# Kernel optimization log

Hardware: AMD Instinct MI355X
Metric: run time of the kernel (lower is better)

Reference implementation:

```python
import jax, jax.numpy as jnp
import numpy as np

B = 131072
D = 256  # embedding_dim
P = 64   # prosody / accent feature dim

# per-speaker prosody constants from the hardcoded 4-speaker table
PITCH_TAB = jnp.array([120.0, 100.0, 220.0, 190.0], dtype=jnp.float32) / 200.0
ENERGY_TAB = jnp.array([0.8, 0.6, 0.85, 0.7], dtype=jnp.float32)
RATE_TAB = jnp.array([1.1, 0.9, 1.15, 1.0], dtype=jnp.float32)


def setup_inputs() -> dict:
    key = jax.random.key(0)
    ks = jax.random.split(key, 16)
    s = 0.05
    return {
        "speaker_id": jax.random.randint(ks[0], (B,), 0, 4, dtype=jnp.int64),
        "emotion_embedding": jax.random.normal(ks[1], (B, D), dtype=jnp.float32),
        "accent_level": 1,
        "emb_table": jax.random.normal(ks[2], (4, D), dtype=jnp.float32),
        "pitch_w": jax.random.normal(ks[3], (P,), dtype=jnp.float32) * s,
        "pitch_b": jax.random.normal(ks[4], (P,), dtype=jnp.float32) * s,
        "energy_w": jax.random.normal(ks[5], (P,), dtype=jnp.float32) * s,
        "energy_b": jax.random.normal(ks[6], (P,), dtype=jnp.float32) * s,
        "rate_w": jax.random.normal(ks[7], (P,), dtype=jnp.float32) * s,
        "rate_b": jax.random.normal(ks[8], (P,), dtype=jnp.float32) * s,
        "accent_table": jax.random.normal(ks[9], (3, P), dtype=jnp.float32),
        "w1": jax.random.normal(ks[10], (D + 3 * P + P, D), dtype=jnp.float32) * s,
        "b1": jnp.zeros((D,), dtype=jnp.float32),
        "ln_g": jnp.ones((D,), dtype=jnp.float32),
        "ln_b": jnp.zeros((D,), dtype=jnp.float32),
        "w2": jax.random.normal(ks[11], (D, D), dtype=jnp.float32) * s,
        "b2": jnp.zeros((D,), dtype=jnp.float32),
        "emo_w": jax.random.normal(ks[12], (D, D), dtype=jnp.float32) * s,
        "emo_b": jnp.zeros((D,), dtype=jnp.float32),
    }


def reference(speaker_id, emotion_embedding, accent_level, emb_table,
              pitch_w, pitch_b, energy_w, energy_b, rate_w, rate_b,
              accent_table, w1, b1, ln_g, ln_b, w2, b2, emo_w, emo_b):
    b = speaker_id.shape[0]
    speaker_embed = emb_table[speaker_id]  # [B, D]
    # vectorized replacement of the per-sample prosody loop: Linear(1,64) == outer product
    pitch_feat = PITCH_TAB[speaker_id][:, None] * pitch_w[None, :] + pitch_b
    energy_feat = ENERGY_TAB[speaker_id][:, None] * energy_w[None, :] + energy_b
    rate_feat = RATE_TAB[speaker_id][:, None] * rate_w[None, :] + rate_b
    prosody = jnp.concatenate([pitch_feat, energy_feat, rate_feat], axis=1)  # [B, 192]
    accent_embed = jnp.broadcast_to(accent_table[accent_level][None, :], (b, P))
    combined = jnp.concatenate([speaker_embed, prosody, accent_embed], axis=1)  # [B, 512]
    h = jax.nn.relu(combined @ w1 + b1)
    # LayerNorm (eps=1e-5)
    mu = jnp.mean(h, axis=-1, keepdims=True)
    var = jnp.mean(jnp.square(h - mu), axis=-1, keepdims=True)
    h = (h - mu) * jax.lax.rsqrt(var + 1e-5) * ln_g + ln_b
    out = h @ w2 + b2
    out = out + 0.3 * (emotion_embedding @ emo_w + emo_b)
    # F.normalize(dim=-1)
    norm = jnp.maximum(jnp.linalg.norm(out, axis=-1, keepdims=True), 1e-12)
    return out / norm
```

## Files before the change

### kernel.cpp

```cpp
#include <hip/hip_runtime.h>
#include <hip/hip_bf16.h>

typedef __attribute__((ext_vector_type(8))) short bf16x8;
typedef __attribute__((ext_vector_type(4))) float f32x4;

static __device__ inline short f2bf(float f) {
    __hip_bfloat16 h = __float2bfloat16(f);
    return *reinterpret_cast<short*>(&h);
}

__global__ __launch_bounds__(1024) void setup_kernel(
    const float* __restrict__ emb_table,
    const float* __restrict__ pitch_w, const float* __restrict__ pitch_b,
    const float* __restrict__ energy_w, const float* __restrict__ energy_b,
    const float* __restrict__ rate_w, const float* __restrict__ rate_b,
    const float* __restrict__ accent_table, const int* __restrict__ accent_level,
    const float* __restrict__ w1, const float* __restrict__ b1,
    const float* __restrict__ ln_g, const float* __restrict__ ln_b,
    const float* __restrict__ w2, const float* __restrict__ b2,
    const float* __restrict__ emo_w, const float* __restrict__ emo_b,
    float* __restrict__ base_out, unsigned short* __restrict__ wpack)
{
    if (blockIdx.x < 4) {
        const int s = blockIdx.x;
        __shared__ float comb[512];
        __shared__ float part[4][256];
        __shared__ float redS[16];
        __shared__ float redQ[16];
        __shared__ float hbuf[256];
        const int t = threadIdx.x;
        const int n = t & 255;
        const int kp = t >> 8;

        if (t < 512) {
            const int i = t;
            float v;
            if (i < 256) {
                v = emb_table[s * 256 + i];
            } else if (i < 320) {
                float pt = (s == 0) ? 0.6f : (s == 1) ? 0.5f : (s == 2) ? 1.1f : 0.95f;
                v = pt * pitch_w[i - 256] + pitch_b[i - 256];
            } else if (i < 384) {
                float et = (s == 0) ? 0.8f : (s == 1) ? 0.6f : (s == 2) ? 0.85f : 0.7f;
                v = et * energy_w[i - 320] + energy_b[i - 320];
            } else if (i < 448) {
                float rt = (s == 0) ? 1.1f : (s == 1) ? 0.9f : (s == 2) ? 1.15f : 1.0f;
                v = rt * rate_w[i - 384] + rate_b[i - 384];
            } else {
                v = accent_table[accent_level[0] * 64 + (i - 448)];
            }
            comb[i] = v;
        }
        __syncthreads();

        float hp = 0.f;
        {
            const int k0 = kp * 128;
            #pragma unroll 8
            for (int k = 0; k < 128; ++k)
                hp = fmaf(comb[k0 + k], w1[(size_t)(k0 + k) * 256 + n], hp);
        }
        part[kp][n] = hp;
        __syncthreads();

        float h = b1[n] + part[0][n] + part[1][n] + part[2][n] + part[3][n];
        h = fmaxf(h, 0.f);

        float sum = h, sq = h * h;
        for (int m = 32; m; m >>= 1) {
            sum += __shfl_xor(sum, m, 64);
            sq  += __shfl_xor(sq, m, 64);
        }
        if ((t & 63) == 0) { redS[t >> 6] = sum; redQ[t >> 6] = sq; }
        __syncthreads();
        const float tot = redS[0] + redS[1] + redS[2] + redS[3];
        const float tsq = redQ[0] + redQ[1] + redQ[2] + redQ[3];
        const float mu  = tot * (1.0f / 256.0f);
        const float var = tsq * (1.0f / 256.0f) - mu * mu;
        const float hn = (h - mu) * rsqrtf(var + 1e-5f) * ln_g[n] + ln_b[n];
        if (t < 256) hbuf[n] = hn;
        __syncthreads();

        float op = 0.f;
        {
            const int k0 = kp * 64;
            #pragma unroll 8
            for (int k = 0; k < 64; ++k)
                op = fmaf(hbuf[k0 + k], w2[(size_t)(k0 + k) * 256 + n], op);
        }
        part[kp][n] = op;
        __syncthreads();
        if (t < 256) {
            base_out[s * 256 + n] = b2[n] + 0.3f * emo_b[n]
                                  + part[0][n] + part[1][n] + part[2][n] + part[3][n];
        }
    } else {
        const int idx = (blockIdx.x - 4) * 1024 + threadIdx.x;
        const int l  = idx & 63;
        const int ks = (idx >> 6) & 7;
        const int ct = idx >> 9;
        const int col = ct * 16 + (l & 15);
        const int kb  = ks * 32 + (l >> 4) * 8;
        bf16x8 pk;
        #pragma unroll
        for (int j = 0; j < 8; ++j) pk[j] = f2bf(emo_w[(size_t)(kb + j) * 256 + col]);
        *reinterpret_cast<bf16x8*>(wpack + (size_t)idx * 8) = pk;
    }
}

__global__ __launch_bounds__(1024) void main_kernel(
    const float* __restrict__ emo, const int* __restrict__ sid,
    const float* __restrict__ base, const unsigned short* __restrict__ wpack,
    float* __restrict__ out)
{
    extern __shared__ unsigned short sB[];
    const int tid = threadIdx.x;

    #pragma unroll
    for (int p = 0; p < 8; ++p) {
        const int e = p * 1024 + tid;
        *reinterpret_cast<bf16x8*>(sB + e * 8) =
            *reinterpret_cast<const bf16x8*>(wpack + (size_t)e * 8);
    }
    __syncthreads();

    const int wave = tid >> 6;
    const int lane = tid & 63;
    const int row0 = blockIdx.x * 256 + wave * 16;
    const int arow = lane & 15;
    const int agrp = lane >> 4;

    const float* aptr = emo + (size_t)(row0 + arow) * 256 + agrp * 8;
    const unsigned short* bptr = sB + lane * 8;

    f32x4 acc[16];
    const f32x4 zero = {0.f, 0.f, 0.f, 0.f};
    #pragma unroll
    for (int i = 0; i < 16; ++i) acc[i] = zero;

    #pragma unroll
    for (int ks = 0; ks < 8; ++ks) {
        f32x4 a0 = *reinterpret_cast<const f32x4*>(aptr + ks * 32);
        f32x4 a1 = *reinterpret_cast<const f32x4*>(aptr + ks * 32 + 4);
        bf16x8 af;
        af[0] = f2bf(a0[0]); af[1] = f2bf(a0[1]); af[2] = f2bf(a0[2]); af[3] = f2bf(a0[3]);
        af[4] = f2bf(a1[0]); af[5] = f2bf(a1[1]); af[6] = f2bf(a1[2]); af[7] = f2bf(a1[3]);
        #pragma unroll
        for (int ct = 0; ct < 16; ++ct) {
            bf16x8 bfr = *reinterpret_cast<const bf16x8*>(bptr + ((ct * 8 + ks) << 9));
            acc[ct] = __builtin_amdgcn_mfma_f32_16x16x32_bf16(af, bfr, acc[ct], 0, 0, 0);
        }
    }

    int sidv[4];
    #pragma unroll
    for (int j = 0; j < 4; ++j) sidv[j] = sid[row0 + agrp * 4 + j];

    float p[4] = {0.f, 0.f, 0.f, 0.f};
    #pragma unroll
    for (int ct = 0; ct < 16; ++ct) {
        #pragma unroll
        for (int j = 0; j < 4; ++j) {
            float pre = fmaf(0.3f, acc[ct][j], base[sidv[j] * 256 + ct * 16 + arow]);
            acc[ct][j] = pre;
            p[j] = fmaf(pre, pre, p[j]);
        }
    }
    #pragma unroll
    for (int j = 0; j < 4; ++j) {
        p[j] += __shfl_xor(p[j], 1, 64);
        p[j] += __shfl_xor(p[j], 2, 64);
        p[j] += __shfl_xor(p[j], 4, 64);
        p[j] += __shfl_xor(p[j], 8, 64);
        float nrm = fmaxf(sqrtf(p[j]), 1e-12f);
        p[j] = 1.0f / nrm;
    }
    #pragma unroll
    for (int ct = 0; ct < 16; ++ct) {
        #pragma unroll
        for (int j = 0; j < 4; ++j) {
            out[(size_t)(row0 + agrp * 4 + j) * 256 + ct * 16 + arow] = acc[ct][j] * p[j];
        }
    }
}

extern "C" void kernel_launch(void* const* d_in, const int* in_sizes, int n_in,
                              void* d_out, int out_size, void* d_ws, size_t ws_size,
                              hipStream_t stream) {
    const int*   sid          = (const int*)d_in[0];
    const float* emo          = (const float*)d_in[1];
    const int*   accent_level = (const int*)d_in[2];
    const float* emb_table    = (const float*)d_in[3];
    const float* pitch_w      = (const float*)d_in[4];
    const float* pitch_b      = (const float*)d_in[5];
    const float* energy_w     = (const float*)d_in[6];
    const float* energy_b     = (const float*)d_in[7];
    const float* rate_w       = (const float*)d_in[8];
    const float* rate_b       = (const float*)d_in[9];
    const float* accent_table = (const float*)d_in[10];
    const float* w1           = (const float*)d_in[11];
    const float* b1           = (const float*)d_in[12];
    const float* ln_g         = (const float*)d_in[13];
    const float* ln_b         = (const float*)d_in[14];
    const float* w2           = (const float*)d_in[15];
    const float* b2           = (const float*)d_in[16];
    const float* emo_w        = (const float*)d_in[17];
    const float* emo_b        = (const float*)d_in[18];

    float* base = (float*)d_ws;
    unsigned short* wpack = (unsigned short*)((char*)d_ws + 4096);

    const int B = in_sizes[0];

    setup_kernel<<<12, 1024, 0, stream>>>(emb_table, pitch_w, pitch_b, energy_w, energy_b,
                                          rate_w, rate_b, accent_table, accent_level,
                                          w1, b1, ln_g, ln_b, w2, b2, emo_w, emo_b,
                                          base, wpack);
    main_kernel<<<B / 256, 1024, 131072, stream>>>(emo, sid, base, wpack, (float*)d_out);
}
```

Before: 297.6 us.

## Process two row tiles per block with async LDS weight loads

Each block now handles 512 rows in two sequential 256-row passes, so the 128 KB bf16 weight staging into LDS is amortized over twice as many rows. The weight copy uses global_load_lds (direct global-to-LDS) and the first tile's activations are loaded before the barrier so the two transfers overlap. Launch bounds gain an occupancy hint. The second tile's loads are not prefetched during the first tile's compute, so the two passes may stay serialized, and the grid halves to 256 blocks.

```diff
diff --git a/kernel.cpp b/kernel.cpp
--- a/kernel.cpp
+++ b/kernel.cpp
@@ -3,6 +3,8 @@
 
 typedef __attribute__((ext_vector_type(8))) short bf16x8;
 typedef __attribute__((ext_vector_type(4))) float f32x4;
+typedef const __attribute__((address_space(1))) unsigned int* gas_u32p;
+typedef __attribute__((address_space(3))) unsigned int* las_u32p;
 
 static __device__ inline short f2bf(float f) {
     __hip_bfloat16 h = __float2bfloat16(f);
@@ -108,80 +110,104 @@
     }
 }
 
-__global__ __launch_bounds__(1024) void main_kernel(
+__global__ __launch_bounds__(1024, 4) void main_kernel(
     const float* __restrict__ emo, const int* __restrict__ sid,
     const float* __restrict__ base, const unsigned short* __restrict__ wpack,
     float* __restrict__ out)
 {
     extern __shared__ unsigned short sB[];
     const int tid = threadIdx.x;
+    const int wave = tid >> 6;
+    const int lane = tid & 63;
+    const int arow = lane & 15;
+    const int agrp = lane >> 4;
+    const unsigned short* bptr = sB + lane * 8;
 
     #pragma unroll
     for (int p = 0; p < 8; ++p) {
         const int e = p * 1024 + tid;
-        *reinterpret_cast<bf16x8*>(sB + e * 8) =
-            *reinterpret_cast<const bf16x8*>(wpack + (size_t)e * 8);
+        __builtin_amdgcn_global_load_lds((gas_u32p)wpack + e * 4,
+                                         (las_u32p)sB + e * 4, 16, 0, 0);
     }
+
+    auto load_convert = [&](int row0, bf16x8* af) {
+        const float* aptr = emo + (size_t)(row0 + arow) * 256 + agrp * 8;
+        f32x4 t0[8], t1[8];
+        #pragma unroll
+        for (int ks = 0; ks < 8; ++ks) {
+            t0[ks] = *reinterpret_cast<const f32x4*>(aptr + ks * 32);
+            t1[ks] = *reinterpret_cast<const f32x4*>(aptr + ks * 32 + 4);
+        }
+        #pragma unroll
+        for (int ks = 0; ks < 8; ++ks) {
+            af[ks][0] = f2bf(t0[ks][0]); af[ks][1] = f2bf(t0[ks][1]);
+            af[ks][2] = f2bf(t0[ks][2]); af[ks][3] = f2bf(t0[ks][3]);
+            af[ks][4] = f2bf(t1[ks][0]); af[ks][5] = f2bf(t1[ks][1]);
+            af[ks][6] = f2bf(t1[ks][2]); af[ks][7] = f2bf(t1[ks][3]);
+        }
+    };
+
+    auto run_mfma = [&](const bf16x8* af, f32x4* acc) {
+        #pragma unroll
+        for (int ks = 0; ks < 8; ++ks) {
+            #pragma unroll
+            for (int ct = 0; ct < 16; ++ct) {
+                bf16x8 bfr = *reinterpret_cast<const bf16x8*>(bptr + ((ct * 8 + ks) << 9));
+                acc[ct] = __builtin_amdgcn_mfma_f32_16x16x32_bf16(af[ks], bfr, acc[ct], 0, 0, 0);
+            }
+        }
+    };
+
+    auto epilogue = [&](int row0, f32x4* acc) {
+        int sidv[4];
+        #pragma unroll
+        for (int j = 0; j < 4; ++j) sidv[j] = sid[row0 + agrp * 4 + j];
+        float p[4] = {0.f, 0.f, 0.f, 0.f};
+        #pragma unroll
+        for (int ct = 0; ct < 16; ++ct) {
+            #pragma unroll
+            for (int j = 0; j < 4; ++j) {
+                float pre = fmaf(0.3f, acc[ct][j], base[sidv[j] * 256 + ct * 16 + arow]);
+                acc[ct][j] = pre;
+                p[j] = fmaf(pre, pre, p[j]);
+            }
+        }
+        #pragma unroll
+        for (int j = 0; j < 4; ++j) {
+            p[j] += __shfl_xor(p[j], 1, 64);
+            p[j] += __shfl_xor(p[j], 2, 64);
+            p[j] += __shfl_xor(p[j], 4, 64);
+            p[j] += __shfl_xor(p[j], 8, 64);
+            p[j] = 1.0f / fmaxf(sqrtf(p[j]), 1e-12f);
+        }
+        #pragma unroll
+        for (int ct = 0; ct < 16; ++ct) {
+            #pragma unroll
+            for (int j = 0; j < 4; ++j) {
+                out[(size_t)(row0 + agrp * 4 + j) * 256 + ct * 16 + arow] = acc[ct][j] * p[j];
+            }
+        }
+    };
+
+    const int rowbase = blockIdx.x * 512 + wave * 16;
+    const f32x4 zero = {0.f, 0.f, 0.f, 0.f};
+
+    bf16x8 af0[8];
+    load_convert(rowbase, af0);
     __syncthreads();
 
-    const int wave = tid >> 6;
-    const int lane = tid & 63;
-    const int row0 = blockIdx.x * 256 + wave * 16;
-    const int arow = lane & 15;
-    const int agrp = lane >> 4;
-
-    const float* aptr = emo + (size_t)(row0 + arow) * 256 + agrp * 8;
-    const unsigned short* bptr = sB + lane * 8;
-
     f32x4 acc[16];
-    const f32x4 zero = {0.f, 0.f, 0.f, 0.f};
     #pragma unroll
     for (int i = 0; i < 16; ++i) acc[i] = zero;
-
+    run_mfma(af0, acc);
+    epilogue(rowbase, acc);
+
+    bf16x8 af1[8];
+    load_convert(rowbase + 256, af1);
     #pragma unroll
-    for (int ks = 0; ks < 8; ++ks) {
-        f32x4 a0 = *reinterpret_cast<const f32x4*>(aptr + ks * 32);
-        f32x4 a1 = *reinterpret_cast<const f32x4*>(aptr + ks * 32 + 4);
-        bf16x8 af;
-        af[0] = f2bf(a0[0]); af[1] = f2bf(a0[1]); af[2] = f2bf(a0[2]); af[3] = f2bf(a0[3]);
-        af[4] = f2bf(a1[0]); af[5] = f2bf(a1[1]); af[6] = f2bf(a1[2]); af[7] = f2bf(a1[3]);
-        #pragma unroll
-        for (int ct = 0; ct < 16; ++ct) {
-            bf16x8 bfr = *reinterpret_cast<const bf16x8*>(bptr + ((ct * 8 + ks) << 9));
-            acc[ct] = __builtin_amdgcn_mfma_f32_16x16x32_bf16(af, bfr, acc[ct], 0, 0, 0);
-        }
-    }
-
-    int sidv[4];
-    #pragma unroll
-    for (int j = 0; j < 4; ++j) sidv[j] = sid[row0 + agrp * 4 + j];
-
-    float p[4] = {0.f, 0.f, 0.f, 0.f};
-    #pragma unroll
-    for (int ct = 0; ct < 16; ++ct) {
-        #pragma unroll
-        for (int j = 0; j < 4; ++j) {
-            float pre = fmaf(0.3f, acc[ct][j], base[sidv[j] * 256 + ct * 16 + arow]);
-            acc[ct][j] = pre;
-            p[j] = fmaf(pre, pre, p[j]);
-        }
-    }
-    #pragma unroll
-    for (int j = 0; j < 4; ++j) {
-        p[j] += __shfl_xor(p[j], 1, 64);
-        p[j] += __shfl_xor(p[j], 2, 64);
-        p[j] += __shfl_xor(p[j], 4, 64);
-        p[j] += __shfl_xor(p[j], 8, 64);
-        float nrm = fmaxf(sqrtf(p[j]), 1e-12f);
-        p[j] = 1.0f / nrm;
-    }
-    #pragma unroll
-    for (int ct = 0; ct < 16; ++ct) {
-        #pragma unroll
-        for (int j = 0; j < 4; ++j) {
-            out[(size_t)(row0 + agrp * 4 + j) * 256 + ct * 16 + arow] = acc[ct][j] * p[j];
-        }
-    }
+    for (int i = 0; i < 16; ++i) acc[i] = zero;
+    run_mfma(af1, acc);
+    epilogue(rowbase + 256, acc);
 }
 
 extern "C" void kernel_launch(void* const* d_in, const int* in_sizes, int n_in,
@@ -216,5 +242,5 @@
                                           rate_w, rate_b, accent_table, accent_level,
                                           w1, b1, ln_g, ln_b, w2, b2, emo_w, emo_b,
                                           base, wpack);
-    main_kernel<<<B / 256, 1024, 131072, stream>>>(emo, sid, base, wpack, (float*)d_out);
-}
+    main_kernel<<<B / 512, 1024, 131072, stream>>>(emo, sid, base, wpack, (float*)d_out);
+}
```

Result: slower. 310.8 us (+4.4%).
